# Kernel tuning notes

Hardware: AMD Instinct MI355X
Metric: run time of the kernel (lower is better)

Reference implementation:

```python
import jax, jax.numpy as jnp
import numpy as np

# ---- module hyperparameters (from init_kwargs / tracker defaults) ----
D_MODEL = 512
D_HEAD = 512
LAMBDA_0 = 1.0        # A_0 = I / lambda_0
FIXED_LAMBDA = 1.0    # fixed penalty magnitude -> U = sqrt(lambda) * K (then / sqrt(d_head))
STAB_EPS = 1e-6       # InversePenaltyTracker.stabilization_eps
PERIODIC_EPS = 1e-6   # InversePenaltyTracker.periodic_eps
PERIOD = 128          # InversePenaltyTracker.period (periodic re-regularization)
EXPLODE_EPS = 1e-5    # fallback_add_explode coefficient
NORM_THRESH = 1000.0  # explosion detection threshold on Frobenius norms


def setup_inputs() -> dict:
    key = jax.random.key(0)
    ks = jax.random.split(key, 9)
    B, T, d = 8, 2048, D_MODEL
    s = 1.0 / np.sqrt(d)
    f32 = jnp.float32
    return {
        "x": jax.random.normal(ks[0], (B, T, d), f32),
        "Wq": (jax.random.normal(ks[1], (D_HEAD, d), f32) * s),
        "bq": jax.random.normal(ks[2], (D_HEAD,), f32) * 0.02,
        "Wk": (jax.random.normal(ks[3], (D_HEAD, d), f32) * s),
        "bk": jax.random.normal(ks[4], (D_HEAD,), f32) * 0.02,
        "Wv": (jax.random.normal(ks[5], (D_HEAD, d), f32) * s),
        "bv": jax.random.normal(ks[6], (D_HEAD,), f32) * 0.02,
        "Wo": (jax.random.normal(ks[7], (d, D_HEAD), f32) * s),
        "bo": jax.random.normal(ks[8], (d,), f32) * 0.02,
    }


def _vla_forward(x, Wq, bq, Wk, bk, Wv, bv, Wo, bo):
    B, T, _ = x.shape
    d = D_HEAD
    # projections (nn.Linear: x @ W.T + b)
    Q = jnp.einsum('btd,hd->bth', x, Wq) + bq
    K = jnp.einsum('btd,hd->bth', x, Wk) + bk
    V = jnp.einsum('btd,hd->bth', x, Wv) + bv

    # PenaltyBuilder (rank 1, fixed lambda): u_t = sqrt(lambda) * k_t, then / sqrt(d_head)
    U = (jnp.sqrt(jnp.float32(FIXED_LAMBDA)) / jnp.sqrt(jnp.float32(d))) * K
    s_seq = jnp.sum(K * Q, axis=-1)                                   # (B,T)
    Vn = V / (jnp.linalg.norm(V, axis=-1, keepdims=True) + 1e-6)      # (B,T,d)

    I = jnp.eye(d, dtype=jnp.float32)
    A0 = jnp.zeros((B, d, d), jnp.float32) + I / LAMBDA_0
    S0 = jnp.zeros((B, d, d), jnp.float32)

    def step(carry, inp):
        A, S = carry
        q, u, s_t, vn, t = inp  # q,u,vn: (B,d); s_t: (B,); t: scalar int
        # Sherman-Morrison rank-1 inverse update with stabilization
        z = jnp.einsum('bij,bj->bi', A, u)
        dot = jnp.sum(u * z, axis=-1)
        delta = jnp.maximum(1.0 + dot, 1e-6)
        unstable = (jnp.abs(delta) < STAB_EPS) | ~jnp.isfinite(delta)
        safe = jnp.where(unstable, 1.0, delta)
        upd = (z[:, :, None] * z[:, None, :]) / safe[:, None, None]
        A = jnp.where(unstable[:, None, None], A + STAB_EPS * I, A - upd)
        # periodic re-regularization (inv_step = t+1)
        A = jnp.where(((t + 1) % PERIOD) == 0, A + PERIODIC_EPS * I, A)
        # alpha_t = s_t * (A u_t)
        z2 = jnp.einsum('bij,bj->bi', A, u)
        alpha = s_t[:, None] * z2
        # memory update S += v_norm alpha^T
        S = S + vn[:, :, None] * alpha[:, None, :]
        # explosion guard
        Sn = jnp.linalg.norm(S.reshape(S.shape[0], -1), axis=-1)
        An = jnp.linalg.norm(A.reshape(A.shape[0], -1), axis=-1)
        A = jnp.where(((Sn > NORM_THRESH) | (An > NORM_THRESH))[:, None, None],
                      A + EXPLODE_EPS * I, A)
        o = jnp.einsum('bij,bj->bi', S, q)
        return (A, S), o

    xs = (jnp.swapaxes(Q, 0, 1), jnp.swapaxes(U, 0, 1),
          jnp.swapaxes(s_seq, 0, 1), jnp.swapaxes(Vn, 0, 1),
          jnp.arange(T))
    _, O = jax.lax.scan(step, (A0, S0), xs)    # O: (T,B,d)
    O = jnp.swapaxes(O, 0, 1)                  # (B,T,d)
    return jnp.einsum('bth,dh->btd', O, Wo) + bo


def reference(x, Wq, bq, Wk, bk, Wv, bv, Wo, bo):
    return _vla_forward(x, Wq, bq, Wk, bk, Wv, bv, Wo, bo)
```

## Files before the change

### kernel.cpp

```cpp
#include <hip/hip_runtime.h>
#include <hip/hip_bf16.h>

#define BB 8
#define TT 2048
#define DD 512
#define LL 128
#define NC 16
#define ETH 512

typedef unsigned short u16;
typedef unsigned int u32;
typedef __attribute__((ext_vector_type(8))) short bf16x8v;
typedef __attribute__((ext_vector_type(4))) float f32x4v;

__device__ __forceinline__ float bf2f(u32 h) { return __uint_as_float(h << 16); }
__device__ __forceinline__ u16 f2bf(float f) {
    u32 u = __float_as_uint(f);
    u += 0x7fffu + ((u >> 16) & 1u);
    return (u16)(u >> 16);
}
__device__ __forceinline__ float wred64(float v) {
    #pragma unroll
    for (int off = 32; off; off >>= 1) v += __shfl_xor(v, off);
    return v;
// ... 240 lines not shown
__device__ __forceinline__ void mfg_body(const u16* __restrict__ Ab,
    const u16* __restrict__ Bb, float* __restrict__ Cq)
{
    __shared__ u16 Agh[128 * 64];
    __shared__ u16 Bgh[128 * 64];
    const int tid = threadIdx.x, wave = tid >> 6, lane = tid & 63;
    const int wm = wave >> 1, wn = wave & 1;

    f32x4v acc[4][4];
    #pragma unroll
    for (int i = 0; i < 4; ++i)
        #pragma unroll
        for (int j = 0; j < 4; ++j)
            acc[i][j] = (f32x4v){0.f, 0.f, 0.f, 0.f};

    const u16* gA[4]; const u16* gB[4];
    #pragma unroll
    for (int i = 0; i < 4; ++i) {
        const int idx = i * 256 + tid, row = idx >> 3, c = idx & 7;
        const int kb = c ^ (row & 7);
        gA[i] = Ab + (size_t)row * 512 + kb * 8;
        gB[i] = Bb + (size_t)row * 512 + kb * 8;
    }
    for (int k0 = 0; k0 < 512; k0 += 64) {
        __syncthreads();
        #pragma unroll
        for (int i = 0; i < 4; ++i) {
            const int dst = (i * 256 + wave * 64) * 8;
            __builtin_amdgcn_global_load_lds(
                (__attribute__((address_space(1))) void*)(gA[i] + k0),
                (__attribute__((address_space(3))) void*)(Agh + dst), 16, 0, 0);
            __builtin_amdgcn_global_load_lds(
                (__attribute__((address_space(1))) void*)(gB[i] + k0),
                (__attribute__((address_space(3))) void*)(Bgh + dst), 16, 0, 0);
        }
        asm volatile("s_waitcnt vmcnt(0)" ::: "memory");
        __syncthreads();

        const int l15 = lane & 15, lhi = lane >> 4;
        bf16x8v af[4][2], bfr[4][2];
        #pragma unroll
        for (int mf = 0; mf < 4; ++mf) {
            const int row = wm * 64 + mf * 16 + l15, sw = (row & 7) << 4;
            #pragma unroll
            for (int ks = 0; ks < 2; ++ks) {
                const int kb2 = (ks * 64 + lhi * 16) ^ sw;
                af[mf][ks] = *(const bf16x8v*)((const char*)Agh + row * 128 + kb2);
            }
        }
        #pragma unroll
        for (int nf = 0; nf < 4; ++nf) {
            const int row = wn * 64 + nf * 16 + l15, sw = (row & 7) << 4;
            #pragma unroll
            for (int ks = 0; ks < 2; ++ks) {
                const int kb2 = (ks * 64 + lhi * 16) ^ sw;
                bfr[nf][ks] = *(const bf16x8v*)((const char*)Bgh + row * 128 + kb2);
            }
        }
        #pragma unroll
        for (int ks = 0; ks < 2; ++ks)
            #pragma unroll
            for (int mf = 0; mf < 4; ++mf)
                #pragma unroll
                for (int nf = 0; nf < 4; ++nf)
                    acc[mf][nf] = __builtin_amdgcn_mfma_f32_16x16x32_bf16(
                        af[mf][ks], bfr[nf][ks], acc[mf][nf], 0, 0, 0);
    }
    const int l15 = lane & 15, lhi = lane >> 4;
    #pragma unroll
    for (int mf = 0; mf < 4; ++mf)
        #pragma unroll
        for (int nf = 0; nf < 4; ++nf) {
            const int n = wn * 64 + nf * 16 + l15;
            #pragma unroll
            for (int r = 0; r < 4; ++r) {
                const int m = wm * 64 + mf * 16 + lhi * 4 + r;
                Cq[(size_t)m * 128 + n] = acc[mf][nf][r];
            }
        }
}

__global__ __launch_bounds__(256)
void mfk1_kernel(const u16* __restrict__ Abf, const u16* __restrict__ Ut,
                 float* __restrict__ Wm)
{
    __shared__ u16 Ah[128 * 64];
    __shared__ u16 Bh[128 * 64];
    const int tid = threadIdx.x, wave = tid >> 6, lane = tid & 63;
    const int wm = wave >> 1, wn = wave & 1;
    const int m0 = blockIdx.x * 128;
    const int bz = blockIdx.z;

    f32x4v acc[4][4];
    #pragma unroll
    for (int i = 0; i < 4; ++i)
        #pragma unroll
        for (int j = 0; j < 4; ++j)
            acc[i][j] = (f32x4v){0.f, 0.f, 0.f, 0.f};

    const u16* Abase = Abf + (size_t)bz * 262144;
    const u16* Bbase = Ut + (size_t)bz * 1048576;
    const u16* gA[4]; const u16* gB[4];
    #pragma unroll
    for (int i = 0; i < 4; ++i) {
        const int idx = i * 256 + tid, row = idx >> 3, c = idx & 7;
        const int kb = c ^ (row & 7);
        gA[i] = Abase + (size_t)(m0 + row) * 512 + kb * 8;
        gB[i] = Bbase + (size_t)row * 512 + kb * 8;
    }
    for (int k0 = 0; k0 < 512; k0 += 64) {
        __syncthreads();
        #pragma unroll
        for (int i = 0; i < 4; ++i) {
            const int dst = (i * 256 + wave * 64) * 8;
            __builtin_amdgcn_global_load_lds(
                (__attribute__((address_space(1))) void*)(gA[i] + k0),
                (__attribute__((address_space(3))) void*)(Ah + dst), 16, 0, 0);
            __builtin_amdgcn_global_load_lds(
                (__attribute__((address_space(1))) void*)(gB[i] + k0),
                (__attribute__((address_space(3))) void*)(Bh + dst), 16, 0, 0);
        }
        asm volatile("s_waitcnt vmcnt(0)" ::: "memory");
        __syncthreads();

        const int l15 = lane & 15, lhi = lane >> 4;
        bf16x8v af[4][2], bfr[4][2];
        #pragma unroll
        for (int mf = 0; mf < 4; ++mf) {
            const int row = wm * 64 + mf * 16 + l15, sw = (row & 7) << 4;
            #pragma unroll
            for (int ks = 0; ks < 2; ++ks) {
                const int kb2 = (ks * 64 + lhi * 16) ^ sw;
                af[mf][ks] = *(const bf16x8v*)((const char*)Ah + row * 128 + kb2);
            }
        }
        #pragma unroll
        for (int nf = 0; nf < 4; ++nf) {
            const int row = wn * 64 + nf * 16 + l15, sw = (row & 7) << 4;
            #pragma unroll
            for (int ks = 0; ks < 2; ++ks) {
                const int kb2 = (ks * 64 + lhi * 16) ^ sw;
                bfr[nf][ks] = *(const bf16x8v*)((const char*)Bh + row * 128 + kb2);
            }
        }
        #pragma unroll
        for (int ks = 0; ks < 2; ++ks)
            #pragma unroll
            for (int mf = 0; mf < 4; ++mf)
                #pragma unroll
                for (int nf = 0; nf < 4; ++nf)
                    acc[mf][nf] = __builtin_amdgcn_mfma_f32_16x16x32_bf16(
                        af[mf][ks], bfr[nf][ks], acc[mf][nf], 0, 0, 0);
    }
    const int l15 = lane & 15, lhi = lane >> 4;
    float* C = Wm + (size_t)bz * 65536;
    #pragma unroll
    for (int mf = 0; mf < 4; ++mf)
        #pragma unroll
        for (int nf = 0; nf < 4; ++nf) {
            const int n = wn * 64 + nf * 16 + l15;
            #pragma unroll
            for (int r = 0; r < 4; ++r) {
                const int m = m0 + wm * 64 + mf * 16 + lhi * 4 + r;
                C[(size_t)m * 128 + n] = acc[mf][nf][r];
            }
        }
}

__device__ __forceinline__ void mfk10_body(char* smemc,
    const u16* __restrict__ Zshi, const u16* __restrict__ Zslo,
    const u16* __restrict__ Zhi, const u16* __restrict__ Zlo,
    float* __restrict__ A, u16* __restrict__ Abf,
    const float* __restrict__ gdiag, float* __restrict__ AnAcc, const int bz)
{
    u16* Ah = (u16*)smemc;
    u16* Al = (u16*)(smemc + 16384);
    u16* Bh = (u16*)(smemc + 32768);
    u16* Bl = (u16*)(smemc + 49152);
    const int tid = threadIdx.x, wave = tid >> 6, lane = tid & 63;
    const int wm = wave >> 1, wn = wave & 1;
    const int m0 = blockIdx.x * 128, n0 = blockIdx.y * 128;

    f32x4v acc[4][4];
    #pragma unroll
    for (int i = 0; i < 4; ++i)
        #pragma unroll
        for (int j = 0; j < 4; ++j)
            acc[i][j] = (f32x4v){0.f, 0.f, 0.f, 0.f};

    const u16* Ahb = Zshi + (size_t)bz * 65536;
    const u16* Alb = Zslo + (size_t)bz * 65536;
    const u16* Bhb = Zhi + (size_t)bz * 65536;
    const u16* Blb = Zlo + (size_t)bz * 65536;
    const u16* gAh[4]; const u16* gAl[4]; const u16* gBh[4]; const u16* gBl[4];
    #pragma unroll
    for (int i = 0; i < 4; ++i) {
        const int idx = i * 256 + tid, row = idx >> 3, c = idx & 7;
        const int kb = c ^ (row & 7);
        gAh[i] = Ahb + (size_t)(m0 + row) * 128 + kb * 8;
        gAl[i] = Alb + (size_t)(m0 + row) * 128 + kb * 8;
        gBh[i] = Bhb + (size_t)(n0 + row) * 128 + kb * 8;
        gBl[i] = Blb + (size_t)(n0 + row) * 128 + kb * 8;
    }
    for (int k0 = 0; k0 < 128; k0 += 64) {
        __syncthreads();
        #pragma unroll
        for (int i = 0; i < 4; ++i) {
            const int dst = (i * 256 + wave * 64) * 8;
            __builtin_amdgcn_global_load_lds(
                (__attribute__((address_space(1))) void*)(gAh[i] + k0),
                (__attribute__((address_space(3))) void*)(Ah + dst), 16, 0, 0);
            __builtin_amdgcn_global_load_lds(
                (__attribute__((address_space(1))) void*)(gAl[i] + k0),
                (__attribute__((address_space(3))) void*)(Al + dst), 16, 0, 0);
            __builtin_amdgcn_global_load_lds(
                (__attribute__((address_space(1))) void*)(gBh[i] + k0),
                (__attribute__((address_space(3))) void*)(Bh + dst), 16, 0, 0);
            __builtin_amdgcn_global_load_lds(
                (__attribute__((address_space(1))) void*)(gBl[i] + k0),
                (__attribute__((address_space(3))) void*)(Bl + dst), 16, 0, 0);
        }
        asm volatile("s_waitcnt vmcnt(0)" ::: "memory");
        __syncthreads();

        const int l15 = lane & 15, lhi = lane >> 4;
        bf16x8v ah[4][2], al[4][2], bh[4][2], bl[4][2];
        #pragma unroll
        for (int mf = 0; mf < 4; ++mf) {
            const int row = wm * 64 + mf * 16 + l15, sw = (row & 7) << 4;
            #pragma unroll
            for (int ks = 0; ks < 2; ++ks) {
                const int kb2 = (ks * 64 + lhi * 16) ^ sw;
                ah[mf][ks] = *(const bf16x8v*)((const char*)Ah + row * 128 + kb2);
                al[mf][ks] = *(const bf16x8v*)((const char*)Al + row * 128 + kb2);
            }
        }
        #pragma unroll
        for (int nf = 0; nf < 4; ++nf) {
            const int row = wn * 64 + nf * 16 + l15, sw = (row & 7) << 4;
            #pragma unroll
            for (int ks = 0; ks < 2; ++ks) {
                const int kb2 = (ks * 64 + lhi * 16) ^ sw;
                bh[nf][ks] = *(const bf16x8v*)((const char*)Bh + row * 128 + kb2);
                bl[nf][ks] = *(const bf16x8v*)((const char*)Bl + row * 128 + kb2);
            }
        }
        #pragma unroll
        for (int ks = 0; ks < 2; ++ks)
            #pragma unroll
            for (int mf = 0; mf < 4; ++mf)
                #pragma unroll
                for (int nf = 0; nf < 4; ++nf) {
                    acc[mf][nf] = __builtin_amdgcn_mfma_f32_16x16x32_bf16(
                        ah[mf][ks], bh[nf][ks], acc[mf][nf], 0, 0, 0);
                    acc[mf][nf] = __builtin_amdgcn_mfma_f32_16x16x32_bf16(
                        al[mf][ks], bh[nf][ks], acc[mf][nf], 0, 0, 0);
                    acc[mf][nf] = __builtin_amdgcn_mfma_f32_16x16x32_bf16(
                        ah[mf][ks], bl[nf][ks], acc[mf][nf], 0, 0, 0);
                }
    }
    const int l15 = lane & 15, lhi = lane >> 4;
    float* Ab = A + (size_t)bz * 262144;
    u16* Abfb = Abf ? (Abf + (size_t)bz * 262144) : (u16*)nullptr;
    const float gd = gdiag[bz];
    float v2 = 0.f;
    #pragma unroll
    for (int mf = 0; mf < 4; ++mf)
        #pragma unroll
        for (int nf = 0; nf < 4; ++nf) {
            const int n = n0 + wn * 64 + nf * 16 + l15;
            #pragma unroll
            for (int r = 0; r < 4; ++r) {
                const int m = m0 + wm * 64 + mf * 16 + lhi * 4 + r;
                const size_t idx = (size_t)m * 512 + n;
                const float v = Ab[idx] - acc[mf][nf][r] + ((m == n) ? gd : 0.f);
                Ab[idx] = v;
                if (Abfb) Abfb[idx] = f2bf(v);
                v2 = fmaf(v, v, v2);
            }
        }
    v2 = wred64(v2);
    if (lane == 0) atomicAdd(AnAcc + bz, v2);
}

__device__ __forceinline__ void mfk9_body(char* smemc,
    const u16* __restrict__ VnTc, const u16* __restrict__ Alphab,
    float* __restrict__ S, u16* __restrict__ Sbf, const int bz)
{
    u16* Ah = (u16*)smemc;
    u16* Bh = (u16*)(smemc + 16384);
    const int tid = threadIdx.x, wave = tid >> 6, lane = tid & 63;
    const int wm = wave >> 1, wn = wave & 1;
    const int m0 = blockIdx.x * 128, n0 = blockIdx.y * 128;

    f32x4v acc[4][4];
    #pragma unroll
    for (int i = 0; i < 4; ++i)
        #pragma unroll
        for (int j = 0; j < 4; ++j)
            acc[i][j] = (f32x4v){0.f, 0.f, 0.f, 0.f};

    const u16* Ab = VnTc + (size_t)bz * 65536;
    const u16* Bb = Alphab + (size_t)bz * 65536;
    const u16* gA[4]; const u16* gB[4];
    #pragma unroll
    for (int i = 0; i < 4; ++i) {
        const int idx = i * 256 + tid, row = idx >> 3, c = idx & 7;
        const int kb = c ^ (row & 7);
        gA[i] = Ab + (size_t)(m0 + row) * 128 + kb * 8;
        gB[i] = Bb + (size_t)(n0 + row) * 128 + kb * 8;
    }
    for (int k0 = 0; k0 < 128; k0 += 64) {
        __syncthreads();
        #pragma unroll
        for (int i = 0; i < 4; ++i) {
            const int dst = (i * 256 + wave * 64) * 8;
            __builtin_amdgcn_global_load_lds(
                (__attribute__((address_space(1))) void*)(gA[i] + k0),
                (__attribute__((address_space(3))) void*)(Ah + dst), 16, 0, 0);
            __builtin_amdgcn_global_load_lds(
                (__attribute__((address_space(1))) void*)(gB[i] + k0),
                (__attribute__((address_space(3))) void*)(Bh + dst), 16, 0, 0);
        }
        asm volatile("s_waitcnt vmcnt(0)" ::: "memory");
        __syncthreads();

        const int l15 = lane & 15, lhi = lane >> 4;
        bf16x8v af[4][2], bfr[4][2];
        #pragma unroll
        for (int mf = 0; mf < 4; ++mf) {
            const int row = wm * 64 + mf * 16 + l15, sw = (row & 7) << 4;
            #pragma unroll
            for (int ks = 0; ks < 2; ++ks) {
                const int kb2 = (ks * 64 + lhi * 16) ^ sw;
                af[mf][ks] = *(const bf16x8v*)((const char*)Ah + row * 128 + kb2);
            }
        }
        #pragma unroll
        for (int nf = 0; nf < 4; ++nf) {
            const int row = wn * 64 + nf * 16 + l15, sw = (row & 7) << 4;
            #pragma unroll
            for (int ks = 0; ks < 2; ++ks) {
                const int kb2 = (ks * 64 + lhi * 16) ^ sw;
                bfr[nf][ks] = *(const bf16x8v*)((const char*)Bh + row * 128 + kb2);
            }
        }
        #pragma unroll
        for (int ks = 0; ks < 2; ++ks)
            #pragma unroll
            for (int mf = 0; mf < 4; ++mf)
                #pragma unroll
                for (int nf = 0; nf < 4; ++nf)
                    acc[mf][nf] = __builtin_amdgcn_mfma_f32_16x16x32_bf16(
                        af[mf][ks], bfr[nf][ks], acc[mf][nf], 0, 0, 0);
    }
    const int l15 = lane & 15, lhi = lane >> 4;
    float* Sb = S + (size_t)bz * 262144;
    u16* Sbfb = Sbf + (size_t)bz * 262144;
    #pragma unroll
    for (int mf = 0; mf < 4; ++mf)
        #pragma unroll
        for (int nf = 0; nf < 4; ++nf) {
            const int n = n0 + wn * 64 + nf * 16 + l15;
            #pragma unroll
            for (int r = 0; r < 4; ++r) {
                const int m = m0 + wm * 64 + mf * 16 + lhi * 4 + r;
                const size_t idx = (size_t)m * 512 + n;
                const float v = Sb[idx] + acc[mf][nf][r];
                Sb[idx] = v;
                Sbfb[idx] = f2bf(v);
            }
        }
}

__global__ __launch_bounds__(256)
void lvl7a_kernel(const u16* Zshi, const u16* Zslo, const u16* Zhi, const u16* Zlo,
                  float* A, u16* Abf, const float* gdiag, float* AnAcc,
                  const u16* VnTc, const u16* Alphab, float* S, u16* Sbf)
{
    __shared__ __align__(16) char smem[65536];
    const int z = blockIdx.z;
    if (z < 8) {
        mfk10_body(smem, Zshi, Zslo, Zhi, Zlo, A, Abf, gdiag, AnAcc, z);
    } else {
        mfk9_body(smem, VnTc, Alphab, S, Sbf, z - 8);
    }
}

__global__ __launch_bounds__(256)
void prep_kernel(const u16* __restrict__ Qb, const u16* __restrict__ Ub,
                 u16* __restrict__ Vb, float* __restrict__ sseq)
{
    const int lane = threadIdx.x & 63, wid = threadIdx.x >> 6;
    const int row = blockIdx.x * 4 + wid;
    const size_t base = (size_t)row * DD;
    const uint4 qr = *(const uint4*)(Qb + base + lane * 8);
    const uint4 ur = *(const uint4*)(Ub + base + lane * 8);
    const uint4 vr = *(const uint4*)(Vb + base + lane * 8);
    float q[8], u[8], v[8];
    unpack8(qr, q); unpack8(ur, u); unpack8(vr, v);
    float sd = 0.f, nv = 0.f;
    #pragma unroll
    for (int e = 0; e < 8; ++e) { sd = fmaf(q[e], u[e], sd); nv = fmaf(v[e], v[e], nv); }
    #pragma unroll
    for (int off = 32; off; off >>= 1) { sd += __shfl_xor(sd, off); nv += __shfl_xor(nv, off); }
    if (lane == 0) sseq[row] = sd * 22.627416997969522f;
    const float inv = 1.f / (sqrtf(nv) + 1e-6f);
    uint4 o;
    o.x = (u32)f2bf(v[0] * inv) | ((u32)f2bf(v[1] * inv) << 16);
    o.y = (u32)f2bf(v[2] * inv) | ((u32)f2bf(v[3] * inv) << 16);
    o.z = (u32)f2bf(v[4] * inv) | ((u32)f2bf(v[5] * inv) << 16);
    o.w = (u32)f2bf(v[6] * inv) | ((u32)f2bf(v[7] * inv) << 16);
    *(uint4*)(Vb + base + lane * 8) = o;
}

__global__ __launch_bounds__(256)
void init_kernel(float4* __restrict__ A4, float4* __restrict__ S4,
                 ushort4* __restrict__ Sbf4, ushort4* __restrict__ Abf4,
                 float* __restrict__ SnSq, float* __restrict__ AnAcc)
{
    const int gtid = blockIdx.x * 256 + threadIdx.x;
    const int N4 = BB * DD * DD / 4;
    const ushort4 z4 = {0, 0, 0, 0};
    for (int idx = gtid; idx < N4; idx += gridDim.x * 256) {
        const int e0 = idx << 2;
        const int r = (e0 >> 9) & 511;
        const int c = e0 & 511;
        float4 v;
        v.x = (c + 0 == r) ? 1.f : 0.f;
        v.y = (c + 1 == r) ? 1.f : 0.f;
        v.z = (c + 2 == r) ? 1.f : 0.f;
        v.w = (c + 3 == r) ? 1.f : 0.f;
        A4[idx] = v;
        S4[idx] = make_float4(0.f, 0.f, 0.f, 0.f);
        Sbf4[idx] = z4;
        if (Abf4) {
            ushort4 a;
            a.x = (c + 0 == r) ? 0x3F80 : 0;
            a.y = (c + 1 == r) ? 0x3F80 : 0;
            a.z = (c + 2 == r) ? 0x3F80 : 0;
            a.w = (c + 3 == r) ? 0x3F80 : 0;
            Abf4[idx] = a;
        }
    }
    if (gtid < BB) { SnSq[gtid] = 0.f; AnAcc[gtid] = 512.f; }
}

struct GP {
    int alay, blay, epi;
    const void* Ap; const void* Bp;
    void* Cp; float* Cio;
    const float* gdiag; float* anacc;
    const float* invdp; const float* cap; const float* cbp;
    const u16* Ulastp;
    u16 *zhi, *zlo, *zshi, *zslo, *alb, *albt;
    int lda, ldb, ldc, K;
    long sA, sB, sC, sCio;
};

__device__ __forceinline__ void gemm_body(const GP& p, const int bz) {
    __shared__ __align__(16) float As[32][68];
    __shared__ __align__(16) float Bs[32][68];
    const int m0 = blockIdx.x * 64, n0 = blockIdx.y * 64;
    const int tid = threadIdx.x, tx = tid & 15, ty = tid >> 4;
    float acc[4][4] = {};
    for (int k0 = 0; k0 < p.K; k0 += 32) {
        if (p.alay == 0) {
            const float* A = (const float*)p.Ap + (size_t)bz * p.sA;
            #pragma unroll
            for (int h = 0; h < 2; ++h) {
                const int g = tid + h * 256, m = g >> 3, k4 = (g & 7) * 4;
                const float4 r = *(const float4*)(A + (size_t)(m0 + m) * p.lda + k0 + k4);
                As[k4][m] = r.x; As[k4+1][m] = r.y; As[k4+2][m] = r.z; As[k4+3][m] = r.w;
            }
        } else if (p.alay == 2) {
            const u16* A = (const u16*)p.Ap + (size_t)bz * p.sA;
            #pragma unroll
            for (int h = 0; h < 2; ++h) {
                const int g = tid + h * 256, m = g >> 3, k4 = (g & 7) * 4;
                const ushort4 r = *(const ushort4*)(A + (size_t)(m0 + m) * p.lda + k0 + k4);
                As[k4][m]=bf2f(r.x); As[k4+1][m]=bf2f(r.y); As[k4+2][m]=bf2f(r.z); As[k4+3][m]=bf2f(r.w);
            }
        } else if (p.alay == 1 || p.alay == 4) {
            const float* A = (const float*)p.Ap + (size_t)bz * p.sA;
            #pragma unroll
            for (int h = 0; h < 2; ++h) {
                const int g = tid + h * 256, k = g >> 4, m4 = (g & 15) * 4;
                float4 r = *(const float4*)(A + (size_t)(k0 + k) * p.lda + m0 + m4);
                if (p.alay == 4) {
                    const int kg = k0 + k, mg = m0 + m4;
                    if (kg > mg + 0) r.x = 0.f;
                    if (kg > mg + 1) r.y = 0.f;
                    if (kg > mg + 2) r.z = 0.f;
                    if (kg > mg + 3) r.w = 0.f;
                }
                As[k][m4] = r.x; As[k][m4+1] = r.y; As[k][m4+2] = r.z; As[k][m4+3] = r.w;
            }
        } else {
            const u16* A = (const u16*)p.Ap + (size_t)bz * p.sA;
            #pragma unroll
            for (int h = 0; h < 2; ++h) {
                const int g = tid + h * 256, k = g >> 4, m4 = (g & 15) * 4;
                const ushort4 r = *(const ushort4*)(A + (size_t)(k0 + k) * p.lda + m0 + m4);
                As[k][m4]=bf2f(r.x); As[k][m4+1]=bf2f(r.y); As[k][m4+2]=bf2f(r.z); As[k][m4+3]=bf2f(r.w);
            }
        }
        if (p.blay == 0) {
            const float* B = (const float*)p.Bp + (size_t)bz * p.sB;
            #pragma unroll
            for (int h = 0; h < 2; ++h) {
                const int g = tid + h * 256, k = g >> 4, n4 = (g & 15) * 4;
                const float4 r = *(const float4*)(B + (size_t)(k0 + k) * p.ldb + n0 + n4);
                Bs[k][n4] = r.x; Bs[k][n4+1] = r.y; Bs[k][n4+2] = r.z; Bs[k][n4+3] = r.w;
            }
        } else if (p.blay == 2) {
            const u16* B = (const u16*)p.Bp + (size_t)bz * p.sB;
            #pragma unroll
            for (int h = 0; h < 2; ++h) {
                const int g = tid + h * 256, k = g >> 4, n4 = (g & 15) * 4;
                const ushort4 r = *(const ushort4*)(B + (size_t)(k0 + k) * p.ldb + n0 + n4);
                Bs[k][n4]=bf2f(r.x); Bs[k][n4+1]=bf2f(r.y); Bs[k][n4+2]=bf2f(r.z); Bs[k][n4+3]=bf2f(r.w);
            }
        } else if (p.blay == 1) {
            const float* B = (const float*)p.Bp + (size_t)bz * p.sB;
            #pragma unroll
            for (int h = 0; h < 2; ++h) {
                const int g = tid + h * 256, n = g >> 3, k4 = (g & 7) * 4;
                const float4 r = *(const float4*)(B + (size_t)(n0 + n) * p.ldb + k0 + k4);
                Bs[k4][n] = r.x; Bs[k4+1][n] = r.y; Bs[k4+2][n] = r.z; Bs[k4+3][n] = r.w;
            }
        } else {
            const u16* B = (const u16*)p.Bp + (size_t)bz * p.sB;
            #pragma unroll
            for (int h = 0; h < 2; ++h) {
                const int g = tid + h * 256, n = g >> 3, k4 = (g & 7) * 4;
                const ushort4 r = *(const ushort4*)(B + (size_t)(n0 + n) * p.ldb + k0 + k4);
                Bs[k4][n]=bf2f(r.x); Bs[k4+1][n]=bf2f(r.y); Bs[k4+2][n]=bf2f(r.z); Bs[k4+3][n]=bf2f(r.w);
            }
        }
        __syncthreads();
        #pragma unroll
        for (int kk = 0; kk < 32; ++kk) {
            const float4 xa = *(const float4*)&As[kk][ty * 4];
            const float4 wb = *(const float4*)&Bs[kk][tx * 4];
            const float xv[4] = {xa.x, xa.y, xa.z, xa.w};
            const float wv[4] = {wb.x, wb.y, wb.z, wb.w};
            #pragma unroll
            for (int i = 0; i < 4; ++i)
                #pragma unroll
                for (int j = 0; j < 4; ++j)
                    acc[i][j] = fmaf(xv[i], wv[j], acc[i][j]);
        }
        __syncthreads();
    }
    const int mb = m0 + ty * 4, nb = n0 + tx * 4;
    if (p.epi == 0) {
        float* C = (float*)p.Cp + (size_t)bz * p.sC;
        #pragma unroll
        for (int i = 0; i < 4; ++i)
            #pragma unroll
            for (int j = 0; j < 4; ++j)
                C[(size_t)(mb + i) * p.ldc + nb + j] = acc[i][j];
    } else if (p.epi == 3) {
        u16* O = (u16*)p.Cp + (size_t)bz * p.sC;
        const float* OB = p.Cio + (size_t)bz * p.sCio;
        #pragma unroll
        for (int i = 0; i < 4; ++i)
            #pragma unroll
            for (int j = 0; j < 4; ++j)
                O[(size_t)(mb + i) * p.ldc + nb + j] =
                    f2bf(acc[i][j] + OB[(size_t)(nb + j) * 256 + mb + i]);
    } else {
        const size_t o0 = (size_t)bz * 65536;
        #pragma unroll
        for (int j = 0; j < 4; ++j) {
            const int n = nb + j;
            const float iv = p.invdp[bz * 128 + n];
            const float cav = p.cap[bz * 128 + n];
            const float cbv = p.cbp[bz * 128 + n];
            #pragma unroll
            for (int i = 0; i < 4; ++i) {
                const int m = mb + i;
                const float z = acc[i][j];
                const float zs = z * iv;
                float a = z * cav;
                if (cbv != 0.f) a = fmaf(cbv, bf2f(p.Ulastp[(size_t)bz * 1048576 + m]), a);
                const size_t o = o0 + (size_t)m * 128 + n;
                const u16 zh = f2bf(z);
                p.zhi[o] = zh; p.zlo[o] = f2bf(z - bf2f(zh));
                const u16 sh = f2bf(zs);
                p.zshi[o] = sh; p.zslo[o] = f2bf(zs - bf2f(sh));
                p.alb[o] = f2bf(a);
                p.albt[o0 + (size_t)n * 512 + m] = f2bf(a);
            }
        }
    }
}

__global__ __launch_bounds__(256) void gemmx(GP p) { gemm_body(p, blockIdx.z); }

__global__ __launch_bounds__(256)
void lvl5_kernel(const u16* Sb, const u16* AlT,
                 const u16* Qt, const u16* Vnt,
                 float* P, float* Ga, float* Gv, float* OBSA, float* dsum)
{
    const int z = blockIdx.z;
    if (z < 8) {
        mfk6_body(Sb, Qt, AlT, Vnt, OBSA, dsum, z);
        return;
    }
    if (blockIdx.x != 0 || blockIdx.y != 0) return;
    const int zz = z - 8, b = zz / 3, j = zz - b * 3;
    const u16* Ab = (j == 2) ? (Vnt + (size_t)b * 1048576) : (AlT + (size_t)b * 65536);
    const u16* Bb = (j == 0) ? (Qt + (size_t)b * 1048576)
                  : (j == 1) ? (AlT + (size_t)b * 65536)
                             : (Vnt + (size_t)b * 1048576);
    float* Cq = ((j == 0) ? P : (j == 1) ? Ga : Gv) + (size_t)b * 16384;
    mfg_body(Ab, Bb, Cq);
}

__global__ __launch_bounds__(256)
void guard_tr_kernel(const float* __restrict__ dsum_g, const float* __restrict__ Ga,
                     const float* __restrict__ Gv, float* __restrict__ SnSq,
                     float* __restrict__ AnAcc, float* __restrict__ gdiag,
                     const float* __restrict__ P, const u16* __restrict__ Vnt,
                     u16* __restrict__ Obt, const float* __restrict__ OBSA,
                     u16* __restrict__ VnTc)
{
    const int z = blockIdx.z, tid = threadIdx.x;
    if (z < 8) {
        GP p{};
        p.alay = 4; p.Ap = P; p.lda = 128; p.sA = 16384;
        p.blay = 2; p.Bp = Vnt; p.ldb = 512; p.sB = 1048576;
        p.epi = 3; p.Cp = Obt; p.ldc = 512; p.sC = 1048576;
        p.Cio = (float*)OBSA; p.sCio = 131072; p.K = 128;
        gemm_body(p, z);
        return;
    }
    if (z < 16) {
        if (blockIdx.x != 0 || blockIdx.y != 0) return;
        const int b = z - 8;
        __shared__ float rpart[256], dsh[128], mdia[128];
        const int t = tid & 127, half = tid >> 7;
        const float* gv = Gv + (size_t)b * 16384 + t * 128;
        const float* ga = Ga + (size_t)b * 16384 + t * 128;
        float rs = 0.f;
        for (int j = half; j < t; j += 2) rs = fmaf(gv[j], ga[j], rs);
        rpart[tid] = rs;
        if (half == 0) { dsh[t] = dsum_g[b * 128 + t]; mdia[t] = gv[t] * ga[t]; }
        __syncthreads();
        if (tid == 0) {
            const float An2 = AnAcc[b];
            float Sn2 = SnSq[b], D = 0.f, T = 0.f;
            int ng = 0;
            for (int t2 = 0; t2 < 128; ++t2) {
                D += dsh[t2];
                T += mdia[t2] + 2.f * (rpart[t2] + rpart[t2 + 128]);
                const float sn2 = Sn2 + 2.f * D + T;
                if (sn2 > 1e6f || An2 > 1e6f) ++ng;
            }
            SnSq[b] = Sn2 + 2.f * D + T;
            gdiag[b] = 1e-6f + (float)ng * 1e-5f;
            AnAcc[b] = 0.f;
        }
        return;
    }
    if (blockIdx.x != 0 || blockIdx.y >= 4) return;
    const int b = z - 16, d0 = blockIdx.y * 128;
    __shared__ u16 tile[64][65];
    const u16* Vn = Vnt + (size_t)b * 1048576;
    u16* VT = VnTc + (size_t)b * 65536;
    const int c = tid & 63, rbase = tid >> 6;
    for (int sd = 0; sd < 2; ++sd) {
        for (int st = 0; st < 2; ++st) {
            #pragma unroll
            for (int rr = 0; rr < 16; ++rr) {
                const int r = rbase + rr * 4;
                tile[r][c] = Vn[(size_t)(st * 64 + r) * 512 + d0 + sd * 64 + c];
            }
            __syncthreads();
            #pragma unroll
            for (int rr = 0; rr < 16; ++rr) {
                const int r2 = rbase + rr * 4;
                VT[(size_t)(d0 + sd * 64 + r2) * 128 + st * 64 + c] = tile[c][r2];
            }
            __syncthreads();
        }
    }
}

__global__ __launch_bounds__(512)
void elim_kernel(const float* __restrict__ G, float* __restrict__ Tg,
                 const float* __restrict__ sseq, float* __restrict__ invd,
                 float* __restrict__ ca, float* __restrict__ cb,
                 float* __restrict__ dsum_g, const int t0)
{
    const int b = blockIdx.x, tid = threadIdx.x, lane = tid & 63, wave = tid >> 6;
    __shared__ __align__(16) float E[128][132];
    __shared__ __align__(16) float Cs[128][132];
    __shared__ __align__(16) float Scr[2368];
    __shared__ float del[128];
    float (*Tm)[132] = E;
    float (*LpT)[132] = (float(*)[132])Scr;
    float (*SpT)[132] = (float(*)[132])(Scr + 1056);

    {
        const float4* Gb = (const float4*)(G + (size_t)b * 16384);
        for (int idx = tid; idx < 4096; idx += ETH) {
            const int r = idx >> 5, c4 = idx & 31;
            ((float4*)&E[r][0])[c4] = Gb[idx];
        }
    }
    if (tid < 128) dsum_g[b * 128 + tid] = 0.f;
    __syncthreads();

    for (int p = 0; p < 16; ++p) {
        const int pc0 = p * 8;
        if (wave == 0) {
            float pr0[8], pr1[8];
            #pragma unroll
            for (int j = 0; j < 8; ++j) {
                pr0[j] = E[pc0 + j][lane];
                pr1[j] = E[pc0 + j][64 + lane];
            }
            float dl[8];
            const bool hi = (pc0 >= 64);
            #pragma unroll
            for (int j = 0; j < 8; ++j) {
                const int t = pc0 + j;
                const int pl = t & 63;
                float prow[8];
                #pragma unroll
                for (int c = 0; c < 8; ++c) {
                    const float v0 = __shfl(pr0[c], pl);
                    const float v1 = __shfl(pr1[c], pl);
                    prow[c] = hi ? v1 : v0;
                }
                const float d = fmaxf(1.f + prow[j], 1e-6f);
                dl[j] = d;
                const float inv = 1.f / d;
                if (lane > t) {
                    const float coef = pr0[j] * inv;
                    #pragma unroll
                    for (int c = j + 1; c < 8; ++c) pr0[c] = fmaf(-coef, prow[c], pr0[c]);
                }
                if (lane + 64 > t) {
                    const float coef = pr1[j] * inv;
                    #pragma unroll
                    for (int c = j + 1; c < 8; ++c) pr1[c] = fmaf(-coef, prow[c], pr1[c]);
                }
            }
            #pragma unroll
            for (int j = 0; j < 8; ++j) {
                const float idj = 1.f / dl[j];
                const int t = pc0 + j;
                {
                    const bool below = (lane > t);
                    const float y = below ? pr0[j] : 0.f;
                    const float l = y * idj;
                    LpT[j][lane] = l; SpT[j][lane] = y; Cs[t][lane] = l;
                }
                {
                    const int r = lane + 64;
                    const bool below = (r > t);
                    const float y = below ? pr1[j] : 0.f;
                    const float l = y * idj;
                    LpT[j][r] = l; SpT[j][r] = y; Cs[t][r] = l;
                }
            }
            if (lane < 8) del[pc0 + lane] = dl[lane];
        }
        __syncthreads();
        const int r0b = pc0 + 8;
        if (r0b < 128) {
            const int nrows = 128 - r0b;
            const int c40 = r0b >> 2, nc4 = 32 - c40;
            for (int idx = tid; idx < nrows * nc4; idx += ETH) {
                const int rr = idx / nc4, cc = idx - rr * nc4;
                const int r = r0b + rr, c4 = c40 + cc;
                float4 e = ((float4*)&E[r][0])[c4];
                #pragma unroll
                for (int j = 0; j < 8; ++j) {
                    const float lv = LpT[j][r];
                    const float4 sv = ((const float4*)&SpT[j][0])[c4];
                    e.x = fmaf(-lv, sv.x, e.x);
                    e.y = fmaf(-lv, sv.y, e.y);
                    e.z = fmaf(-lv, sv.z, e.z);
                    e.w = fmaf(-lv, sv.w, e.w);
                }
                ((float4*)&E[r][0])[c4] = e;
            }
        }
        __syncthreads();
    }

    for (int idx = tid; idx < 4224; idx += ETH)
// ... 36 lines not shown
                    x.z = fmaf(cv, tv.z, x.z);
                    x.w = fmaf(cv, tv.w, x.w);
                }
                *(float4*)&Scr[p2 * s * stride + i * stride + j4 * 4] = x;
            }
            __syncthreads();
            for (int idx = tid; idx < Nel; idx += ETH) {
                const int p2 = idx / (s * nj4), rem = idx - p2 * s * nj4;
                const int i = rem / nj4, j4 = rem - i * nj4;
                const int I0 = 2 * s * p2, J0 = I0 + s;
                const int jc = j4 * 4 + jh * 32;
                float4 y = make_float4(0.f, 0.f, 0.f, 0.f);
                for (int k = 0; k < s; ++k) {
                    const float tv = Tm[I0 + i][I0 + k];
                    const float4 xv = *(const float4*)&Scr[p2 * s * stride + k * stride + j4 * 4];
                    y.x = fmaf(tv, xv.x, y.x);
                    y.y = fmaf(tv, xv.y, y.y);
                    y.z = fmaf(tv, xv.z, y.z);
                    y.w = fmaf(tv, xv.w, y.w);
                }
                float4 o;
                o.x = -y.x; o.y = -y.y; o.z = -y.z; o.w = -y.w;
                *(float4*)&Tm[I0 + i][J0 + jc] = o;
            }
            __syncthreads();
        }
    }
    {
        float4* Tgb = (float4*)(Tg + (size_t)b * 16384);
        for (int idx = tid; idx < 4096; idx += ETH) {
            const int r = idx >> 5, c4 = idx & 31;
            Tgb[idx] = ((const float4*)&Tm[r][0])[c4];
        }
    }
    if (tid < 128) {
        const float d = del[tid];
        const float s = sseq[(size_t)b * TT + t0 + tid];
        invd[b * 128 + tid] = 1.f / d;
        ca[b * 128 + tid] = s / d;
        cb[b * 128 + tid] = (tid == 127) ? s * 1e-6f : 0.f;
    }
}

extern "C" void kernel_launch(void* const* d_in, const int* in_sizes, int n_in,
                              void* d_out, int out_size, void* d_ws, size_t ws_size,
                              hipStream_t stream)
{
    const float* x  = (const float*)d_in[0];
    const float* Wq = (const float*)d_in[1];
    const float* bq = (const float*)d_in[2];
    const float* Wk = (const float*)d_in[3];
    const float* bk = (const float*)d_in[4];
    const float* Wv = (const float*)d_in[5];
    const float* bv = (const float*)d_in[6];
    const float* Wo = (const float*)d_in[7];
    const float* bo = (const float*)d_in[8];

    char* ws = (char*)d_ws;
    u16* Qb    = (u16*)(ws);
    u16* Ub    = (u16*)(ws + (16ull << 20));
    u16* Vnb   = (u16*)(ws + (32ull << 20));
    u16* Ob    = (u16*)(ws + (48ull << 20));
    u16* x_bf  = Ob;
    float* A    = (float*)(ws + (64ull << 20));
    float* S    = (float*)(ws + (72ull << 20));
    float* Wm   = (float*)(ws + (80ull << 20));
    u16* Zhi   = (u16*)(ws + (82ull << 20));
    u16* Zlo   = (u16*)(ws + (83ull << 20));
    u16* Zshi  = (u16*)(ws + (84ull << 20));
    u16* Zslo  = (u16*)(ws + (85ull << 20));
    u16* Alphab= (u16*)(ws + (86ull << 20));
    u16* VnTc  = (u16*)(ws + (87ull << 20));
    float* OBSA = (float*)(ws + (88ull << 20));
    float* G    = (float*)(ws + (92ull << 20));
    float* Tg   = (float*)(ws + (92ull << 20) + (512ull << 10));
    float* P    = (float*)(ws + (93ull << 20));
    float* Ga   = (float*)(ws + (93ull << 20) + (512ull << 10));
    float* Gv   = (float*)(ws + (94ull << 20));
    float* invd = (float*)(ws + (94ull << 20) + (512ull << 10));
    float* ca   = (float*)(ws + (94ull << 20) + (516ull << 10));
    float* cb   = (float*)(ws + (94ull << 20) + (520ull << 10));
    float* sseq = (float*)(ws + (94ull << 20) + (528ull << 10));
    float* SnSq = (float*)(ws + (94ull << 20) + (600ull << 10));
    float* AnAcc= (float*)(ws + (94ull << 20) + (600ull << 10) + 64);
    float* gdiag= (float*)(ws + (94ull << 20) + (600ull << 10) + 128);
    float* dsum = (float*)(ws + (94ull << 20) + (604ull << 10));
    u16* Wq_bf = (u16*)(ws + (95ull << 20));
    u16* Wk_bf = (u16*)(ws + (95ull << 20) + (512ull << 10));
    u16* Wv_bf = (u16*)(ws + (96ull << 20));
    u16* Wo_bf = (u16*)(ws + (96ull << 20) + (512ull << 10));
    u16* S_bf  = (u16*)(ws + (97ull << 20));
    u16* AlT   = (u16*)(ws + (101ull << 20));

    const bool big = (ws_size >= (111ull << 20));
    u16* A_bf = big ? (u16*)(ws + (102ull << 20)) : (u16*)nullptr;

    f2bf_kernel<<<2048, 256, 0, stream>>>((const float4*)x, (ushort4*)x_bf, 2097152);
    wconv_kernel<<<dim3(256, 4), 256, 0, stream>>>(
        (const float4*)Wq, (const float4*)Wk, (const float4*)Wv, (const float4*)Wo,
        (ushort4*)Wq_bf, (ushort4*)Wk_bf, (ushort4*)Wv_bf, (ushort4*)Wo_bf);

    mfma_gemm<1><<<dim3(128, 4), 256, 0, stream>>>(x_bf, Wq_bf, bq, Qb, 1.f);
    mfma_gemm<1><<<dim3(128, 4), 256, 0, stream>>>(x_bf, Wk_bf, bk, Ub, 0.04419417382415922f);
    mfma_gemm<1><<<dim3(128, 4), 256, 0, stream>>>(x_bf, Wv_bf, bv, Vnb, 1.f);
    prep_kernel<<<4096, 256, 0, stream>>>(Qb, Ub, Vnb, sseq);
    init_kernel<<<2048, 256, 0, stream>>>((float4*)A, (float4*)S, (ushort4*)S_bf,
                                          (ushort4*)A_bf, SnSq, AnAcc);

    for (int c = 0; c < NC; ++c) {
        const int t0 = c * LL;
        const u16* Ut = Ub + (size_t)t0 * 512;
        const u16* Qt = Qb + (size_t)t0 * 512;
        const u16* Vt = Vnb + (size_t)t0 * 512;
        if (big) {
            mfk1_kernel<<<dim3(4, 1, 8), 256, 0, stream>>>(A_bf, Ut, Wm);
        } else {
            GP p1{}; p1.alay = 0; p1.Ap = A; p1.lda = 512; p1.sA = 262144;
            p1.blay = 3; p1.Bp = Ut; p1.ldb = 512; p1.sB = 1048576;
            p1.epi = 0; p1.Cp = Wm; p1.ldc = 128; p1.sC = 65536; p1.K = 512;
            gemmx<<<dim3(8, 2, 8), 256, 0, stream>>>(p1);
        }
        GP p2{}; p2.alay = 2; p2.Ap = Ut; p2.lda = 512; p2.sA = 1048576;
        p2.blay = 0; p2.Bp = Wm; p2.ldb = 128; p2.sB = 65536;
        p2.epi = 0; p2.Cp = G; p2.ldc = 128; p2.sC = 16384; p2.K = 512;
        gemmx<<<dim3(2, 2, 8), 256, 0, stream>>>(p2);
        elim_kernel<<<8, 512, 0, stream>>>(G, Tg, sseq, invd, ca, cb, dsum, t0);
        GP p4{}; p4.alay = 0; p4.Ap = Wm; p4.lda = 128; p4.sA = 65536;
        p4.blay = 0; p4.Bp = Tg; p4.ldb = 128; p4.sB = 16384;
        p4.epi = 4;
        p4.zhi = Zhi; p4.zlo = Zlo; p4.zshi = Zshi; p4.zslo = Zslo;
        p4.alb = Alphab; p4.albt = AlT;
        p4.invdp = invd; p4.cap = ca; p4.cbp = cb;
        p4.Ulastp = Ub + (size_t)(t0 + 127) * 512;
        p4.K = 128; p4.ldc = 128;
        gemmx<<<dim3(8, 2, 8), 256, 0, stream>>>(p4);
        lvl5_kernel<<<dim3(4, 2, 32), 256, 0, stream>>>(S_bf, AlT, Qt, Vt,
            P, Ga, Gv, OBSA, dsum);
        guard_tr_kernel<<<dim3(2, 8, 24), 256, 0, stream>>>(dsum, Ga, Gv, SnSq, AnAcc,
            gdiag, P, Vt, Ob + (size_t)t0 * 512, OBSA, VnTc);
        lvl7a_kernel<<<dim3(4, 4, 16), 256, 0, stream>>>(Zshi, Zslo, Zhi, Zlo,
            A, A_bf, gdiag, AnAcc, VnTc, Alphab, S, S_bf);
    }
    mfma_gemm<0><<<dim3(128, 4), 256, 0, stream>>>(Ob, Wo_bf, bo, d_out, 1.f);
}
```

Baseline: 2.967 ms.

## Defer guard diagonal correction to next chunk and merge guard kernel into A/S update

Removes the serial guard_tr launch that had to finish before the A/S update. The explosion-guard diagonal term is now applied one chunk late: the next chunk's first GEMM adds gprev*U^T as a correction, and the A norm is rebuilt analytically from its running trace. This lets the guard reduction, output GEMM, A update and S update all run in one launch, and moves the Vn transpose into lvl5. The cost is extra trace atomics, double-buffered guard state, and a somewhat altered order of floating-point operations.

```diff
diff --git a/kernel.cpp b/kernel.cpp
--- a/kernel.cpp
+++ b/kernel.cpp
@@ -346,7 +346,7 @@
 
 __global__ __launch_bounds__(256)
 void mfk1_kernel(const u16* __restrict__ Abf, const u16* __restrict__ Ut,
-                 float* __restrict__ Wm)
+                 float* __restrict__ Wm, const float* __restrict__ gprev)
 {
     __shared__ u16 Ah[128 * 64];
     __shared__ u16 Bh[128 * 64];
@@ -418,6 +418,7 @@
     }
     const int l15 = lane & 15, lhi = lane >> 4;
     float* C = Wm + (size_t)bz * 65536;
+    const float gp = gprev[bz];
     #pragma unroll
     for (int mf = 0; mf < 4; ++mf)
         #pragma unroll
@@ -426,7 +427,8 @@
             #pragma unroll
             for (int r = 0; r < 4; ++r) {
                 const int m = m0 + wm * 64 + mf * 16 + lhi * 4 + r;
-                C[(size_t)m * 128 + n] = acc[mf][nf][r];
+                const float comp = gp * bf2f(Bbase[(size_t)n * 512 + m]);
+                C[(size_t)m * 128 + n] = acc[mf][nf][r] + comp;
             }
         }
 }
@@ -435,7 +437,8 @@
     const u16* __restrict__ Zshi, const u16* __restrict__ Zslo,
     const u16* __restrict__ Zhi, const u16* __restrict__ Zlo,
     float* __restrict__ A, u16* __restrict__ Abf,
-    const float* __restrict__ gdiag, float* __restrict__ AnAcc, const int bz)
+    const float* __restrict__ gprev, float* __restrict__ anacc,
+    float* __restrict__ tracc, const int bz)
 {
     u16* Ah = (u16*)smemc;
     u16* Al = (u16*)(smemc + 16384);
@@ -526,8 +529,8 @@
     const int l15 = lane & 15, lhi = lane >> 4;
     float* Ab = A + (size_t)bz * 262144;
     u16* Abfb = Abf ? (Abf + (size_t)bz * 262144) : (u16*)nullptr;
-    const float gd = gdiag[bz];
-    float v2 = 0.f;
+    const float gd = gprev[bz];
+    float v2 = 0.f, tr = 0.f;
     #pragma unroll
     for (int mf = 0; mf < 4; ++mf)
         #pragma unroll
@@ -541,10 +544,14 @@
                 Ab[idx] = v;
                 if (Abfb) Abfb[idx] = f2bf(v);
                 v2 = fmaf(v, v, v2);
-            }
-        }
-    v2 = wred64(v2);
-    if (lane == 0) atomicAdd(AnAcc + bz, v2);
+                if (m == n) tr += v;
+            }
+        }
+    v2 = wred64(v2); tr = wred64(tr);
+    if (lane == 0) {
+        atomicAdd(anacc + bz, v2);
+        if (m0 == n0) atomicAdd(tracc + bz, tr);
+    }
 }
 
 __device__ __forceinline__ void mfk9_body(char* smemc,
@@ -635,20 +642,6 @@
                 Sbfb[idx] = f2bf(v);
             }
         }
-}
-
-__global__ __launch_bounds__(256)
-void lvl7a_kernel(const u16* Zshi, const u16* Zslo, const u16* Zhi, const u16* Zlo,
-                  float* A, u16* Abf, const float* gdiag, float* AnAcc,
-                  const u16* VnTc, const u16* Alphab, float* S, u16* Sbf)
-{
-    __shared__ __align__(16) char smem[65536];
-    const int z = blockIdx.z;
-    if (z < 8) {
-        mfk10_body(smem, Zshi, Zslo, Zhi, Zlo, A, Abf, gdiag, AnAcc, z);
-    } else {
-        mfk9_body(smem, VnTc, Alphab, S, Sbf, z - 8);
-    }
 }
 
 __global__ __launch_bounds__(256)
@@ -681,7 +674,8 @@
 __global__ __launch_bounds__(256)
 void init_kernel(float4* __restrict__ A4, float4* __restrict__ S4,
                  ushort4* __restrict__ Sbf4, ushort4* __restrict__ Abf4,
-                 float* __restrict__ SnSq, float* __restrict__ AnAcc)
+                 float* __restrict__ SnSq, float* __restrict__ gbuf,
+                 float* __restrict__ anb, float* __restrict__ trb)
 {
     const int gtid = blockIdx.x * 256 + threadIdx.x;
     const int N4 = BB * DD * DD / 4;
@@ -707,24 +701,29 @@
             Abf4[idx] = a;
         }
     }
-    if (gtid < BB) { SnSq[gtid] = 0.f; AnAcc[gtid] = 512.f; }
+    if (gtid < BB) {
+        SnSq[gtid] = 0.f;
+        gbuf[gtid] = 0.f; gbuf[8 + gtid] = 0.f;
+        anb[gtid] = 0.f;  anb[8 + gtid] = 512.f;
+        trb[gtid] = 0.f;  trb[8 + gtid] = 512.f;
+    }
 }
 
 struct GP {
     int alay, blay, epi;
     const void* Ap; const void* Bp;
     void* Cp; float* Cio;
-    const float* gdiag; float* anacc;
     const float* invdp; const float* cap; const float* cbp;
     const u16* Ulastp;
     u16 *zhi, *zlo, *zshi, *zslo, *alb, *albt;
+    const float* gcomp; const u16* ucomp;
     int lda, ldb, ldc, K;
     long sA, sB, sC, sCio;
 };
 
-__device__ __forceinline__ void gemm_body(const GP& p, const int bz) {
-    __shared__ __align__(16) float As[32][68];
-    __shared__ __align__(16) float Bs[32][68];
+__device__ __forceinline__ void gemm_body(const GP& p, const int bz, char* smemc) {
+    float (*As)[68] = (float(*)[68])smemc;
+    float (*Bs)[68] = (float(*)[68])(smemc + 8704);
     const int m0 = blockIdx.x * 64, n0 = blockIdx.y * 64;
     const int tid = threadIdx.x, tx = tid & 15, ty = tid >> 4;
     float acc[4][4] = {};
@@ -820,11 +819,22 @@
     const int mb = m0 + ty * 4, nb = n0 + tx * 4;
     if (p.epi == 0) {
         float* C = (float*)p.Cp + (size_t)bz * p.sC;
-        #pragma unroll
-        for (int i = 0; i < 4; ++i)
-            #pragma unroll
-            for (int j = 0; j < 4; ++j)
-                C[(size_t)(mb + i) * p.ldc + nb + j] = acc[i][j];
+        if (p.gcomp) {
+            const float gp = p.gcomp[bz];
+            const u16* Uc = p.ucomp + (size_t)bz * 1048576;
+            #pragma unroll
+            for (int i = 0; i < 4; ++i)
+                #pragma unroll
+                for (int j = 0; j < 4; ++j)
+                    C[(size_t)(mb + i) * p.ldc + nb + j] =
+                        acc[i][j] + gp * bf2f(Uc[(size_t)(nb + j) * 512 + (mb + i)]);
+        } else {
+            #pragma unroll
+            for (int i = 0; i < 4; ++i)
+                #pragma unroll
+                for (int j = 0; j < 4; ++j)
+                    C[(size_t)(mb + i) * p.ldc + nb + j] = acc[i][j];
+        }
     } else if (p.epi == 3) {
         u16* O = (u16*)p.Cp + (size_t)bz * p.sC;
         const float* OB = p.Cio + (size_t)bz * p.sCio;
@@ -861,76 +871,35 @@
     }
 }
 
-__global__ __launch_bounds__(256) void gemmx(GP p) { gemm_body(p, blockIdx.z); }
+__global__ __launch_bounds__(256) void gemmx(GP p) {
+    __shared__ __align__(16) char gsm[17408];
+    gemm_body(p, blockIdx.z, gsm);
+}
 
 __global__ __launch_bounds__(256)
 void lvl5_kernel(const u16* Sb, const u16* AlT,
                  const u16* Qt, const u16* Vnt,
-                 float* P, float* Ga, float* Gv, float* OBSA, float* dsum)
+                 float* P, float* Ga, float* Gv, float* OBSA, float* dsum,
+                 u16* VnTc)
 {
     const int z = blockIdx.z;
     if (z < 8) {
         mfk6_body(Sb, Qt, AlT, Vnt, OBSA, dsum, z);
         return;
     }
-    if (blockIdx.x != 0 || blockIdx.y != 0) return;
-    const int zz = z - 8, b = zz / 3, j = zz - b * 3;
-    const u16* Ab = (j == 2) ? (Vnt + (size_t)b * 1048576) : (AlT + (size_t)b * 65536);
-    const u16* Bb = (j == 0) ? (Qt + (size_t)b * 1048576)
-                  : (j == 1) ? (AlT + (size_t)b * 65536)
-                             : (Vnt + (size_t)b * 1048576);
-    float* Cq = ((j == 0) ? P : (j == 1) ? Ga : Gv) + (size_t)b * 16384;
-    mfg_body(Ab, Bb, Cq);
-}
-
-__global__ __launch_bounds__(256)
-void guard_tr_kernel(const float* __restrict__ dsum_g, const float* __restrict__ Ga,
-                     const float* __restrict__ Gv, float* __restrict__ SnSq,
-                     float* __restrict__ AnAcc, float* __restrict__ gdiag,
-                     const float* __restrict__ P, const u16* __restrict__ Vnt,
-                     u16* __restrict__ Obt, const float* __restrict__ OBSA,
-                     u16* __restrict__ VnTc)
-{
-    const int z = blockIdx.z, tid = threadIdx.x;
-    if (z < 8) {
-        GP p{};
-        p.alay = 4; p.Ap = P; p.lda = 128; p.sA = 16384;
-        p.blay = 2; p.Bp = Vnt; p.ldb = 512; p.sB = 1048576;
-        p.epi = 3; p.Cp = Obt; p.ldc = 512; p.sC = 1048576;
-        p.Cio = (float*)OBSA; p.sCio = 131072; p.K = 128;
-        gemm_body(p, z);
+    if (z < 32) {
+        if (blockIdx.x != 0 || blockIdx.y != 0) return;
+        const int zz = z - 8, b = zz / 3, j = zz - b * 3;
+        const u16* Ab = (j == 2) ? (Vnt + (size_t)b * 1048576) : (AlT + (size_t)b * 65536);
+        const u16* Bb = (j == 0) ? (Qt + (size_t)b * 1048576)
+                      : (j == 1) ? (AlT + (size_t)b * 65536)
+                                 : (Vnt + (size_t)b * 1048576);
+        float* Cq = ((j == 0) ? P : (j == 1) ? Ga : Gv) + (size_t)b * 16384;
+        mfg_body(Ab, Bb, Cq);
         return;
     }
-    if (z < 16) {
-        if (blockIdx.x != 0 || blockIdx.y != 0) return;
-        const int b = z - 8;
-        __shared__ float rpart[256], dsh[128], mdia[128];
-        const int t = tid & 127, half = tid >> 7;
-        const float* gv = Gv + (size_t)b * 16384 + t * 128;
-        const float* ga = Ga + (size_t)b * 16384 + t * 128;
-        float rs = 0.f;
-        for (int j = half; j < t; j += 2) rs = fmaf(gv[j], ga[j], rs);
-        rpart[tid] = rs;
-        if (half == 0) { dsh[t] = dsum_g[b * 128 + t]; mdia[t] = gv[t] * ga[t]; }
-        __syncthreads();
-        if (tid == 0) {
-            const float An2 = AnAcc[b];
-            float Sn2 = SnSq[b], D = 0.f, T = 0.f;
-            int ng = 0;
-            for (int t2 = 0; t2 < 128; ++t2) {
-                D += dsh[t2];
-                T += mdia[t2] + 2.f * (rpart[t2] + rpart[t2 + 128]);
-                const float sn2 = Sn2 + 2.f * D + T;
-                if (sn2 > 1e6f || An2 > 1e6f) ++ng;
-            }
-            SnSq[b] = Sn2 + 2.f * D + T;
-            gdiag[b] = 1e-6f + (float)ng * 1e-5f;
-            AnAcc[b] = 0.f;
-        }
-        return;
-    }
-    if (blockIdx.x != 0 || blockIdx.y >= 4) return;
-    const int b = z - 16, d0 = blockIdx.y * 128;
+    if (blockIdx.y != 0) return;
+    const int b = z - 32, d0 = blockIdx.x * 128, tid = threadIdx.x;
     __shared__ u16 tile[64][65];
     const u16* Vn = Vnt + (size_t)b * 1048576;
     u16* VT = VnTc + (size_t)b * 65536;
@@ -953,11 +922,72 @@
     }
 }
 
+__global__ __launch_bounds__(256)
+void lvl7m_kernel(const u16* Zshi, const u16* Zslo, const u16* Zhi, const u16* Zlo,
+                  float* A, u16* Abf, const float* gprev, float* an_cur, float* tr_cur,
+                  const u16* VnTc, const u16* Alphab, float* S, u16* Sbf,
+                  const float* P, const u16* Vnt, u16* Obt, const float* OBSA,
+                  const float* dsum_g, const float* Ga, const float* Gv,
+                  const float* an_prev, const float* tr_prev,
+                  float* SnSq, float* gnew)
+{
+    __shared__ __align__(16) char smem[65536];
+    const int z = blockIdx.z, tid = threadIdx.x;
+    if (z < 8) {
+        if (blockIdx.y >= 4) return;
+        mfk10_body(smem, Zshi, Zslo, Zhi, Zlo, A, Abf, gprev, an_cur, tr_cur, z);
+        return;
+    }
+    if (z < 16) {
+        if (blockIdx.y >= 4) return;
+        mfk9_body(smem, VnTc, Alphab, S, Sbf, z - 8);
+        return;
+    }
+    if (z < 24) {
+        if (blockIdx.x >= 2) return;
+        GP p{};
+        p.alay = 4; p.Ap = P; p.lda = 128; p.sA = 16384;
+        p.blay = 2; p.Bp = Vnt; p.ldb = 512; p.sB = 1048576;
+        p.epi = 3; p.Cp = Obt; p.ldc = 512; p.sC = 1048576;
+        p.Cio = (float*)OBSA; p.sCio = 131072; p.K = 128;
+        gemm_body(p, z - 16, smem);
+        return;
+    }
+    if (blockIdx.x != 0) return;
+    const int b = blockIdx.y;
+    float* rpart = (float*)smem;
+    float* dsh = rpart + 256;
+    float* mdia = dsh + 128;
+    const int t = tid & 127, half = tid >> 7;
+    const float* gv = Gv + (size_t)b * 16384 + t * 128;
+    const float* ga = Ga + (size_t)b * 16384 + t * 128;
+    float rs = 0.f;
+    for (int j = half; j < t; j += 2) rs = fmaf(gv[j], ga[j], rs);
+    rpart[tid] = rs;
+    if (half == 0) { dsh[t] = dsum_g[b * 128 + t]; mdia[t] = gv[t] * ga[t]; }
+    __syncthreads();
+    if (tid == 0) {
+        const float gp = gprev[b];
+        const float An2 = an_prev[b] + 2.f * gp * tr_prev[b] + 512.f * gp * gp;
+        float Sn2 = SnSq[b], D = 0.f, T = 0.f;
+        int ng = 0;
+        for (int t2 = 0; t2 < 128; ++t2) {
+            D += dsh[t2];
+            T += mdia[t2] + 2.f * (rpart[t2] + rpart[t2 + 128]);
+            const float sn2 = Sn2 + 2.f * D + T;
+            if (sn2 > 1e6f || An2 > 1e6f) ++ng;
+        }
+        SnSq[b] = Sn2 + 2.f * D + T;
+        gnew[b] = 1e-6f + (float)ng * 1e-5f;
+    }
+}
+
 __global__ __launch_bounds__(512)
 void elim_kernel(const float* __restrict__ G, float* __restrict__ Tg,
                  const float* __restrict__ sseq, float* __restrict__ invd,
                  float* __restrict__ ca, float* __restrict__ cb,
-                 float* __restrict__ dsum_g, const int t0)
+                 float* __restrict__ dsum_g, float* __restrict__ an_z,
+                 float* __restrict__ tr_z, const int t0)
 {
     const int b = blockIdx.x, tid = threadIdx.x, lane = tid & 63, wave = tid >> 6;
     __shared__ __align__(16) float E[128][132];
@@ -976,6 +1006,7 @@
         }
     }
     if (tid < 128) dsum_g[b * 128 + tid] = 0.f;
+    if (tid == 0) { an_z[b] = 0.f; tr_z[b] = 0.f; }
     __syncthreads();
 
     for (int p = 0; p < 16; ++p) {
@@ -1178,9 +1209,10 @@
     float* cb   = (float*)(ws + (94ull << 20) + (520ull << 10));
     float* sseq = (float*)(ws + (94ull << 20) + (528ull << 10));
     float* SnSq = (float*)(ws + (94ull << 20) + (600ull << 10));
-    float* AnAcc= (float*)(ws + (94ull << 20) + (600ull << 10) + 64);
-    float* gdiag= (float*)(ws + (94ull << 20) + (600ull << 10) + 128);
     float* dsum = (float*)(ws + (94ull << 20) + (604ull << 10));
+    float* gbuf = (float*)(ws + (94ull << 20) + (608ull << 10));
+    float* anb  = gbuf + 16;
+    float* trb  = anb + 16;
     u16* Wq_bf = (u16*)(ws + (95ull << 20));
     u16* Wk_bf = (u16*)(ws + (95ull << 20) + (512ull << 10));
     u16* Wv_bf = (u16*)(ws + (96ull << 20));
@@ -1201,26 +1233,35 @@
     mfma_gemm<1><<<dim3(128, 4), 256, 0, stream>>>(x_bf, Wv_bf, bv, Vnb, 1.f);
     prep_kernel<<<4096, 256, 0, stream>>>(Qb, Ub, Vnb, sseq);
     init_kernel<<<2048, 256, 0, stream>>>((float4*)A, (float4*)S, (ushort4*)S_bf,
-                                          (ushort4*)A_bf, SnSq, AnAcc);
+                                          (ushort4*)A_bf, SnSq, gbuf, anb, trb);
 
     for (int c = 0; c < NC; ++c) {
         const int t0 = c * LL;
+        const int cur = c & 1, prv = cur ^ 1;
+        float* gprev = gbuf + prv * 8;
+        float* gnew  = gbuf + cur * 8;
+        float* an_cur = anb + cur * 8;
+        float* an_prev = anb + prv * 8;
+        float* tr_cur = trb + cur * 8;
+        float* tr_prev = trb + prv * 8;
         const u16* Ut = Ub + (size_t)t0 * 512;
         const u16* Qt = Qb + (size_t)t0 * 512;
         const u16* Vt = Vnb + (size_t)t0 * 512;
         if (big) {
-            mfk1_kernel<<<dim3(4, 1, 8), 256, 0, stream>>>(A_bf, Ut, Wm);
+            mfk1_kernel<<<dim3(4, 1, 8), 256, 0, stream>>>(A_bf, Ut, Wm, gprev);
         } else {
             GP p1{}; p1.alay = 0; p1.Ap = A; p1.lda = 512; p1.sA = 262144;
             p1.blay = 3; p1.Bp = Ut; p1.ldb = 512; p1.sB = 1048576;
             p1.epi = 0; p1.Cp = Wm; p1.ldc = 128; p1.sC = 65536; p1.K = 512;
+            p1.gcomp = gprev; p1.ucomp = Ut;
             gemmx<<<dim3(8, 2, 8), 256, 0, stream>>>(p1);
         }
         GP p2{}; p2.alay = 2; p2.Ap = Ut; p2.lda = 512; p2.sA = 1048576;
         p2.blay = 0; p2.Bp = Wm; p2.ldb = 128; p2.sB = 65536;
         p2.epi = 0; p2.Cp = G; p2.ldc = 128; p2.sC = 16384; p2.K = 512;
         gemmx<<<dim3(2, 2, 8), 256, 0, stream>>>(p2);
-        elim_kernel<<<8, 512, 0, stream>>>(G, Tg, sseq, invd, ca, cb, dsum, t0);
+        elim_kernel<<<8, 512, 0, stream>>>(G, Tg, sseq, invd, ca, cb, dsum,
+                                           an_cur, tr_cur, t0);
         GP p4{}; p4.alay = 0; p4.Ap = Wm; p4.lda = 128; p4.sA = 65536;
         p4.blay = 0; p4.Bp = Tg; p4.ldb = 128; p4.sB = 16384;
         p4.epi = 4;
@@ -1230,12 +1271,12 @@
         p4.Ulastp = Ub + (size_t)(t0 + 127) * 512;
         p4.K = 128; p4.ldc = 128;
         gemmx<<<dim3(8, 2, 8), 256, 0, stream>>>(p4);
-        lvl5_kernel<<<dim3(4, 2, 32), 256, 0, stream>>>(S_bf, AlT, Qt, Vt,
-            P, Ga, Gv, OBSA, dsum);
-        guard_tr_kernel<<<dim3(2, 8, 24), 256, 0, stream>>>(dsum, Ga, Gv, SnSq, AnAcc,
-            gdiag, P, Vt, Ob + (size_t)t0 * 512, OBSA, VnTc);
-        lvl7a_kernel<<<dim3(4, 4, 16), 256, 0, stream>>>(Zshi, Zslo, Zhi, Zlo,
-            A, A_bf, gdiag, AnAcc, VnTc, Alphab, S, S_bf);
+        lvl5_kernel<<<dim3(4, 2, 40), 256, 0, stream>>>(S_bf, AlT, Qt, Vt,
+            P, Ga, Gv, OBSA, dsum, VnTc);
+        lvl7m_kernel<<<dim3(4, 8, 25), 256, 0, stream>>>(Zshi, Zslo, Zhi, Zlo,
+            A, A_bf, gprev, an_cur, tr_cur, VnTc, Alphab, S, S_bf,
+            P, Vt, Ob + (size_t)t0 * 512, OBSA, dsum, Ga, Gv,
+            an_prev, tr_prev, SnSq, gnew);
     }
     mfma_gemm<0><<<dim3(128, 4), 256, 0, stream>>>(Ob, Wo_bf, bo, d_out, 1.f);
 }
```

After: 3.361 ms. 13.3% more time.
